# Optimization experiments

Measured on AMD Instinct MI355X. Metric: run time of the kernel, lower is better.

Reference implementation:

```python
import jax, jax.numpy as jnp
import numpy as np

DIM = 1024
D_STATE = 64
D_CONV = 4
EXPAND = 2
D_INNER = DIM * EXPAND          # 2048
N_HEADS = D_INNER // 64         # 32
HEAD_DIM = D_INNER // N_HEADS   # 64
B_SZ = 1
SEQ = 1024
D_IN_PROJ = 2 * D_INNER + 2 * D_STATE + N_HEADS  # 4256
EPS = 1e-6


def setup_inputs() -> dict:
    key = jax.random.key(0)
    ks = jax.random.split(key, 9)
    x = jax.random.normal(ks[0], (B_SZ, SEQ, DIM), jnp.float32)
    W_in = jax.random.normal(ks[1], (D_IN_PROJ, DIM), jnp.float32) / np.sqrt(DIM)
    W_conv = jax.random.normal(ks[2], (D_INNER, 1, D_CONV), jnp.float32) / np.sqrt(D_CONV)
    b_conv = 0.01 * jax.random.normal(ks[3], (D_INNER,), jnp.float32)
    # A_log init: log(arange(1..d_state)) broadcast to (h, d, n), as in the module
    A_log = jnp.log(jnp.arange(1, D_STATE + 1, dtype=jnp.float32)) * jnp.ones((N_HEADS, HEAD_DIM, D_STATE), jnp.float32)
    D = jnp.ones((N_HEADS, HEAD_DIM), jnp.float32) + 0.01 * jax.random.normal(ks[4], (N_HEADS, HEAD_DIM), jnp.float32)
    dt_bias = 0.1 * jax.random.normal(ks[5], (N_HEADS,), jnp.float32)
    norm_w = jnp.ones((D_INNER,), jnp.float32) + 0.01 * jax.random.normal(ks[6], (D_INNER,), jnp.float32)
    W_out = jax.random.normal(ks[7], (DIM, D_INNER), jnp.float32) / np.sqrt(D_INNER)
    return {"x": x, "W_in": W_in, "W_conv": W_conv, "b_conv": b_conv,
            "A_log": A_log, "D": D, "dt_bias": dt_bias, "norm_w": norm_w, "W_out": W_out}


def reference(x, W_in, W_conv, b_conv, A_log, D, dt_bias, norm_w, W_out):
    Bsz, L, _ = x.shape
    zxBCdt = x @ W_in.T  # (B, L, D_IN_PROJ)
    z, xin, Bm, Cm, dt = jnp.split(
        zxBCdt,
        [D_INNER, 2 * D_INNER, 2 * D_INNER + D_STATE, 2 * D_INNER + 2 * D_STATE],
        axis=-1)
    # causal depthwise conv1d (padding d_conv-1 then truncate == left-pad d_conv-1)
    xc = jnp.transpose(xin, (0, 2, 1))  # (B, d_inner, L)
    xc = jax.lax.conv_general_dilated(
        xc, W_conv, window_strides=(1,), padding=[(D_CONV - 1, 0)],
        feature_group_count=D_INNER, dimension_numbers=("NCH", "OIH", "NCH"))
    xc = xc + b_conv[None, :, None]
    xin = jax.nn.silu(jnp.transpose(xc, (0, 2, 1)))  # (B, L, d_inner)
    xh = xin.reshape(Bsz, L, N_HEADS, HEAD_DIM)      # (B, L, h, d)

    A = -jnp.exp(A_log)                     # (h, d, n)
    dt = jax.nn.softplus(dt + dt_bias)      # (B, L, h)

    def step(h_state, ins):
        x_t, dt_t, B_t, C_t = ins  # (B,h,d), (B,h), (B,n), (B,n)
        a = jnp.exp(dt_t[:, :, None, None] * A[None])          # (B,h,d,n)
        h_state = a * h_state + B_t[:, None, None, :] * x_t[..., None]
        y_t = jnp.einsum("bhdn,bn->bhd", h_state, C_t)
        return h_state, y_t

    h0 = jnp.zeros((Bsz, N_HEADS, HEAD_DIM, D_STATE), x.dtype)
    xs = (jnp.moveaxis(xh, 1, 0), jnp.moveaxis(dt, 1, 0),
          jnp.moveaxis(Bm, 1, 0), jnp.moveaxis(Cm, 1, 0))
    _, ys = jax.lax.scan(step, h0, xs)
    y = jnp.moveaxis(ys, 0, 1)              # (B, L, h, d)
    y = y + xh * D[None, None]              # skip term
    y = y.reshape(Bsz, L, D_INNER)
    y = y * jax.nn.silu(z)                  # gating
    rms = jnp.sqrt(jnp.mean(y * y, axis=-1, keepdims=True) + EPS)
    y = y / rms * norm_w                    # RMSNorm
    return y @ W_out.T                      # (B, L, dim)
```

## Files before the change

kernel.cpp:

```cpp
#include <hip/hip_runtime.h>

typedef unsigned short u16;
typedef unsigned int u32;
typedef __attribute__((ext_vector_type(8))) short bf16x8;
typedef __attribute__((ext_vector_type(4))) float f32x4;

#define GPTR(p) ((const __attribute__((address_space(1))) void*)(p))
#define SPTR(p) ((__attribute__((address_space(3))) void*)(p))

#define L_SEQ 1024
#define DIM 1024
#define D_INNER 2048
#define D_STATE 64
#define N_HEADS 32
#define NPROJ 4256
#define NPROJ_PAD 4352
#define COL_Z 0
#define COL_X 2048
#define COL_B 4096
#define COL_C 4160
#define COL_DT 4224
#define NCHUNK 32
#define QCH 32

__device__ __forceinline__ u16 f2bf(float f) {
    unsigned int u = __float_as_uint(f);
    u = u + 0x7fffu + ((u >> 16) & 1u);
    return (u16)(u >> 16);
}
__device__ __forceinline__ float bf2f(u16 h) {
    unsigned int u = ((unsigned int)h) << 16;
    return __uint_as_float(u);
}

__global__ __launch_bounds__(256)
void cast_all_kernel(const float* __restrict__ x, const float* __restrict__ W_in,
                     const float* __restrict__ W_out,
                     u16* __restrict__ xb_hi, u16* __restrict__ xb_lo,
                     u16* __restrict__ Winb, u16* __restrict__ Winb_lo,
                     u16* __restrict__ Woutb)
{
    const int b = blockIdx.x;
    if (b < 1024) {
        const int i = (b * 256 + threadIdx.x) * 4;
        const float4 v = *(const float4*)&x[i];
        const float vs[4] = { v.x, v.y, v.z, v.w };
        u16 oh[4], ol[4];
        #pragma unroll
        for (int j = 0; j < 4; ++j) {
            oh[j] = f2bf(vs[j]);
            ol[j] = f2bf(vs[j] - bf2f(oh[j]));
        }
        *(ushort4*)&xb_hi[i] = *(ushort4*)oh;
        *(ushort4*)&xb_lo[i] = *(ushort4*)ol;
    } else if (b < 5376) {
        const int i = ((b - 1024) * 256 + threadIdx.x) * 4;
        float4 v = make_float4(0.f, 0.f, 0.f, 0.f);
        if (i < NPROJ * DIM) v = *(const float4*)&W_in[i];
        u16 o[4] = { f2bf(v.x), f2bf(v.y), f2bf(v.z), f2bf(v.w) };
        *(ushort4*)&Winb[i] = *(ushort4*)o;
    } else if (b < 5632) {
        const int i = ((b - 5376) * 256 + threadIdx.x) * 4;
        float4 v = make_float4(0.f, 0.f, 0.f, 0.f);
        if (i < (NPROJ - 4096) * DIM) v = *(const float4*)&W_in[(size_t)4096 * DIM + i];
        const float vs[4] = { v.x, v.y, v.z, v.w };
        u16 oh[4], ol[4];
        #pragma unroll
        for (int j = 0; j < 4; ++j) {
            oh[j] = f2bf(vs[j]);
            ol[j] = f2bf(vs[j] - bf2f(oh[j]));
        }
        *(ushort4*)&Winb[(size_t)4096 * DIM + i] = *(ushort4*)oh;
        *(ushort4*)&Winb_lo[i] = *(ushort4*)ol;
    } else {
        const int i = ((b - 5632) * 256 + threadIdx.x) * 4;
        const float4 v = *(const float4*)&W_out[i];
        u16 o[4] = { f2bf(v.x), f2bf(v.y), f2bf(v.z), f2bf(v.w) };
        *(ushort4*)&Woutb[i] = *(ushort4*)o;
    }
}

__global__ __launch_bounds__(256, 2)
void gemm_bt128(const u16* __restrict__ Ah, const u16* __restrict__ Al,
                const u16* __restrict__ Bh, const u16* __restrict__ Bl,
                float* __restrict__ C, int K, int ldc, int precise_from)
{
    __shared__ u16 As[128 * 32];
    __shared__ u16 Bs[128 * 32];
    __shared__ u16 AsL[128 * 32];
    __shared__ u16 BsL[128 * 32];
    const int tid  = threadIdx.x;
    const int wave = tid >> 6;
    const int lane = tid & 63;
    const int row0 = blockIdx.y * 128;
    const int col0 = blockIdx.x * 128;
    const int wm = (wave >> 1) * 64;
    const int wn = (wave & 1) * 64;
    const bool precise = ((int)blockIdx.x >= precise_from);

    f32x4 acc[4][4] = {};

    const int r15 = lane & 15;
    const int ko  = (lane >> 4) * 8;

    for (int kt = 0; kt < K; kt += 32) {
        #pragma unroll
        for (int call = 0; call < 2; ++call) {
            const int ob = call * 4096 + wave * 1024 + lane * 16;
            const int rr = ob >> 6;
            const int kk = (ob & 63) >> 1;
            const size_t goff = (size_t)(row0 + rr) * K + kt + kk;
            const size_t gofb = (size_t)(col0 + rr) * K + kt + kk;
            const int lofs = call * 2048 + wave * 512;
            __builtin_amdgcn_global_load_lds(GPTR(Ah + goff), SPTR(As + lofs), 16, 0, 0);
            __builtin_amdgcn_global_load_lds(GPTR(Bh + gofb), SPTR(Bs + lofs), 16, 0, 0);
            if (precise) {
                __builtin_amdgcn_global_load_lds(GPTR(Al + goff), SPTR(AsL + lofs), 16, 0, 0);
                __builtin_amdgcn_global_load_lds(GPTR(Bl + gofb), SPTR(BsL + lofs), 16, 0, 0);
            }
        }
        __syncthreads();
        bf16x8 av[4], bv[4];
        #pragma unroll
        for (int i = 0; i < 4; ++i)
            av[i] = *(const bf16x8*)&As[(wm + i * 16 + r15) * 32 + ko];
        #pragma unroll
        for (int j = 0; j < 4; ++j)
            bv[j] = *(const bf16x8*)&Bs[(wn + j * 16 + r15) * 32 + ko];
        if (precise) {
            bf16x8 avl[4], bvl[4];
            #pragma unroll
            for (int i = 0; i < 4; ++i)
                avl[i] = *(const bf16x8*)&AsL[(wm + i * 16 + r15) * 32 + ko];
            #pragma unroll
            for (int j = 0; j < 4; ++j)
                bvl[j] = *(const bf16x8*)&BsL[(wn + j * 16 + r15) * 32 + ko];
            #pragma unroll
            for (int i = 0; i < 4; ++i)
                #pragma unroll
                for (int j = 0; j < 4; ++j) {
                    acc[i][j] = __builtin_amdgcn_mfma_f32_16x16x32_bf16(av[i],  bv[j],  acc[i][j], 0, 0, 0);
                    acc[i][j] = __builtin_amdgcn_mfma_f32_16x16x32_bf16(av[i],  bvl[j], acc[i][j], 0, 0, 0);
                    acc[i][j] = __builtin_amdgcn_mfma_f32_16x16x32_bf16(avl[i], bv[j],  acc[i][j], 0, 0, 0);
                }
        } else {
            #pragma unroll
            for (int i = 0; i < 4; ++i)
                #pragma unroll
                for (int j = 0; j < 4; ++j)
                    acc[i][j] = __builtin_amdgcn_mfma_f32_16x16x32_bf16(av[i], bv[j], acc[i][j], 0, 0, 0);
        }
        __syncthreads();
    }

    const int cl = lane & 15;
    const int rg = (lane >> 4) * 4;
    #pragma unroll
    for (int i = 0; i < 4; ++i)
        #pragma unroll
        for (int j = 0; j < 4; ++j)
            #pragma unroll
            for (int reg = 0; reg < 4; ++reg) {
                const int rrow = row0 + wm + i * 16 + rg + reg;
                const int ccol = col0 + wn + j * 16 + cl;
                C[(size_t)rrow * ldc + ccol] = acc[i][j][reg];
            }
}

__global__ __launch_bounds__(256, 2)
void gemm_bt128_sk(const u16* __restrict__ Ah, const u16* __restrict__ Bh,
                   float* __restrict__ Cpart, int Kslice, int lda, int ldb, int ldc)
{
    __shared__ u16 As[128 * 32];
    __shared__ u16 Bs[128 * 32];
    const int tid  = threadIdx.x;
    const int wave = tid >> 6;
    const int lane = tid & 63;
    const int row0 = blockIdx.y * 128;
    const int col0 = blockIdx.x * 128;
    const int wm = (wave >> 1) * 64;
    const int wn = (wave & 1) * 64;
    const int kbase = blockIdx.z * Kslice;
    float* Cp = Cpart + (size_t)blockIdx.z * (1024 * 1024);

    f32x4 acc[4][4] = {};
    const int r15 = lane & 15;
    const int ko  = (lane >> 4) * 8;

    for (int kt = kbase; kt < kbase + Kslice; kt += 32) {
        #pragma unroll
        for (int call = 0; call < 2; ++call) {
            const int ob = call * 4096 + wave * 1024 + lane * 16;
            const int rr = ob >> 6;
            const int kk = (ob & 63) >> 1;
            const int lofs = call * 2048 + wave * 512;
            __builtin_amdgcn_global_load_lds(GPTR(Ah + (size_t)(row0 + rr) * lda + kt + kk),
                                             SPTR(As + lofs), 16, 0, 0);
            __builtin_amdgcn_global_load_lds(GPTR(Bh + (size_t)(col0 + rr) * ldb + kt + kk),
                                             SPTR(Bs + lofs), 16, 0, 0);
        }
        __syncthreads();
        bf16x8 av[4], bv[4];
        #pragma unroll
        for (int i = 0; i < 4; ++i)
            av[i] = *(const bf16x8*)&As[(wm + i * 16 + r15) * 32 + ko];
        #pragma unroll
        for (int j = 0; j < 4; ++j)
            bv[j] = *(const bf16x8*)&Bs[(wn + j * 16 + r15) * 32 + ko];
        #pragma unroll
        for (int i = 0; i < 4; ++i)
            #pragma unroll
            for (int j = 0; j < 4; ++j)
                acc[i][j] = __builtin_amdgcn_mfma_f32_16x16x32_bf16(av[i], bv[j], acc[i][j], 0, 0, 0);
        __syncthreads();
    }

    const int cl = lane & 15;
    const int rg = (lane >> 4) * 4;
    #pragma unroll
    for (int i = 0; i < 4; ++i)
        #pragma unroll
        for (int j = 0; j < 4; ++j)
            #pragma unroll
            for (int reg = 0; reg < 4; ++reg)
                Cp[(size_t)(row0 + wm + i * 16 + rg + reg) * ldc + col0 + wn + j * 16 + cl]
                    = acc[i][j][reg];
}

__global__ __launch_bounds__(256)
void reduce4_kernel(const float* __restrict__ Cpart, float* __restrict__ out)
{
    const int i = (blockIdx.x * 256 + threadIdx.x) * 4;
    const float4 a = *(const float4*)&Cpart[i];
    const float4 b = *(const float4*)&Cpart[i + 1024 * 1024];
    const float4 c = *(const float4*)&Cpart[i + 2 * 1024 * 1024];
    const float4 d = *(const float4*)&Cpart[i + 3 * 1024 * 1024];
    *(float4*)&out[i] = make_float4(a.x + b.x + c.x + d.x, a.y + b.y + c.y + d.y,
                                    a.z + b.z + c.z + d.z, a.w + b.w + c.w + d.w);
}

__global__ __launch_bounds__(256)
void conv_dt_kernel(const float* __restrict__ P,
                    const float* __restrict__ Wc,
                    const float* __restrict__ bc,
                    const float* __restrict__ dtb,
                    const float* __restrict__ A_log,
                    float* __restrict__ xconv,
                    float2* __restrict__ BCp2,
                    float* __restrict__ gT,
                    float* __restrict__ decayT)
{
    const int b = blockIdx.x;
    if (b < 1024) {
        const int t = b;
        const int tid = threadIdx.x;
        const int c0 = tid * 8;
        float acc[8];
        #pragma unroll
        for (int j = 0; j < 8; ++j) acc[j] = bc[c0 + j];
        #pragma unroll
        for (int k = 0; k < 4; ++k) {
            const int tt = t - 3 + k;
            if (tt >= 0) {
                const float* row = P + (size_t)tt * NPROJ_PAD + COL_X + c0;
                float4 a0 = *(const float4*)row;
                float4 a1 = *(const float4*)(row + 4);
                float xv[8] = { a0.x, a0.y, a0.z, a0.w, a1.x, a1.y, a1.z, a1.w };
                #pragma unroll
                for (int j = 0; j < 8; ++j)
                    acc[j] = fmaf(xv[j], Wc[(c0 + j) * 4 + k], acc[j]);
            }
        }
        float o[8];
        #pragma unroll
        for (int j = 0; j < 8; ++j) {
            const float v = acc[j];
            o[j] = v / (1.f + __expf(-v));
        }
        float* dst = xconv + (size_t)t * D_INNER + c0;
        *(float4*)dst       = make_float4(o[0], o[1], o[2], o[3]);
        *(float4*)(dst + 4) = make_float4(o[4], o[5], o[6], o[7]);
        if (tid < 64) {
            const float Bv = P[(size_t)t * NPROJ_PAD + COL_B + tid];
            const float Cv = P[(size_t)t * NPROJ_PAD + COL_C + tid];
            BCp2[t * 64 + tid] = make_float2(Bv, Cv);
        }
    } else {
        const int wv = threadIdx.x >> 6;
        const int lane = threadIdx.x & 63;
        const int idx = (b - 1024) * 4 + wv;
        const int h = idx >> 4;
        const int pr = idx & 15;
        const int t0 = pr * 64;
        float v = P[(size_t)(t0 + lane) * NPROJ_PAD + COL_DT + h] + dtb[h];
        v = (v > 15.f) ? v : __logf(1.f + __expf(v));
        float g = v;
        #pragma unroll
        for (int off = 1; off < 32; off <<= 1) {
            const float u = __shfl_up(g, off);
            if ((lane & 31) >= off) g += u;
        }
        gT[h * L_SEQ + t0 + lane] = g;
        const float Av = -__expf(A_log[(size_t)h * 4096 + lane]);
        #pragma unroll 8
        for (int tt = 0; tt < 64; ++tt) {
            const float dtt = __shfl(v, tt);
            decayT[((size_t)h * L_SEQ + t0 + tt) * 64 + lane] = __expf(dtt * Av);
        }
    }
}

__global__ __launch_bounds__(256)
void xpose_kernel(const float* __restrict__ xconv, float* __restrict__ xT)
{
    __shared__ float tile[64][65];
    const int t0 = blockIdx.x * 64;
    const int c0 = blockIdx.y * 64;
    const int lr = threadIdx.x >> 6;
    const int lc = threadIdx.x & 63;
    #pragma unroll
    for (int r = 0; r < 16; ++r) {
        const int row = r * 4 + lr;
        tile[row][lc] = xconv[(size_t)(t0 + row) * D_INNER + c0 + lc];
    }
    __syncthreads();
    #pragma unroll
    for (int r = 0; r < 16; ++r) {
        const int row = r * 4 + lr;
        xT[(size_t)(c0 + row) * L_SEQ + t0 + lc] = tile[lc][row];
    }
}

__global__ __launch_bounds__(128, 4)
void scan_local_kernel(const float2* __restrict__ BCp2,
                       const float* __restrict__ decayT,
                       const float* __restrict__ xT,
                       float* __restrict__ ygt,
                       u16* __restrict__ S)
{
    __shared__ float2 pt[2][8][2][65];
    const int wv = threadIdx.x >> 6;
    const int lane = threadIdx.x & 63;
    const int hd0 = blockIdx.x * 16 + wv * 8;
    const int pr = blockIdx.y;
    const int h = hd0 >> 6;
    const int tb = pr * 64;

    float sA[8] = {0.f,0.f,0.f,0.f,0.f,0.f,0.f,0.f};
    float sB[8] = {0.f,0.f,0.f,0.f,0.f,0.f,0.f,0.f};

    const float2* bcA = BCp2 + (size_t)tb * 64 + lane;
    const float2* bcB = bcA + 32 * 64;
    const float* dAp = decayT + ((size_t)h * L_SEQ + tb) * 64 + lane;
    const float* dBp = dAp + 32 * 64;
    const float* xr0 = xT + (size_t)hd0 * L_SEQ + tb;

    const int r16 = lane & 15;
    const int seg = lane >> 4;
    const int rd = r16 >> 1;
    const int ri = r16 & 1;

    #pragma unroll
    for (int g = 0; g < 8; ++g) {
        float xA[8][4], xB[8][4];
        #pragma unroll
        for (int d = 0; d < 8; ++d) {
            const float* xr = xr0 + d * L_SEQ;
            const float4 a = *(const float4*)(xr + g * 4);
            const float4 b = *(const float4*)(xr + 32 + g * 4);
            xA[d][0]=a.x; xA[d][1]=a.y; xA[d][2]=a.z; xA[d][3]=a.w;
            xB[d][0]=b.x; xB[d][1]=b.y; xB[d][2]=b.z; xB[d][3]=b.w;
        }
        #pragma unroll
        for (int half = 0; half < 2; ++half) {
            #pragma unroll
            for (int ii2 = 0; ii2 < 2; ++ii2) {
                const int ii = half * 2 + ii2;
                const int i = g * 4 + ii;
                const float2 vA = bcA[i * 64];
                const float2 vB = bcB[i * 64];
                const float aA = dAp[i * 64];
                const float aB = dBp[i * 64];
                #pragma unroll
                for (int d = 0; d < 8; ++d) {
                    sA[d] = fmaf(aA, sA[d], vA.x * xA[d][ii]);
                    sB[d] = fmaf(aB, sB[d], vB.x * xB[d][ii]);
                }
                #pragma unroll
                for (int d = 0; d < 8; ++d)
                    pt[wv][d][ii2][lane] = make_float2(sA[d] * vA.y, sB[d] * vB.y);
            }
            float px = 0.f, py = 0.f;
            #pragma unroll
            for (int k = 0; k < 16; ++k) {
                const float2 v = pt[wv][rd][ri][seg * 16 + k];
                px += v.x; py += v.y;
            }
            px += __shfl_xor(px, 16); py += __shfl_xor(py, 16);
            px += __shfl_xor(px, 32); py += __shfl_xor(py, 32);
            if (lane < 16) {
                const int tA = tb + g * 4 + half * 2 + ri;
                ygt[(size_t)tA * D_INNER + hd0 + rd] = px;
                ygt[(size_t)(tA + 32) * D_INNER + hd0 + rd] = py;
            }
        }
    }
    #pragma unroll
    for (int d = 0; d < 8; ++d) {
        S[((size_t)(hd0 + d) * NCHUNK + pr * 2    ) * 64 + lane] = f2bf(sA[d]);
        S[((size_t)(hd0 + d) * NCHUNK + pr * 2 + 1) * 64 + lane] = f2bf(sB[d]);
    }
}

__global__ __launch_bounds__(256)
void chunk_combine_kernel(const float* __restrict__ A_log,
                          const float* __restrict__ gT,
                          u16* __restrict__ S)
{
    const int tid = blockIdx.x * 256 + threadIdx.x;
    const int hd = tid >> 6;
    const int n  = tid & 63;
    const int h  = hd >> 6;
    const float Av = -__expf(A_log[(size_t)hd * 64 + n]);
    float H = 0.f;
    #pragma unroll 8
    for (int c = 0; c < NCHUNK; ++c) {
        const float Gc = gT[h * L_SEQ + c * QCH + QCH - 1];
        const size_t idx = ((size_t)hd * NCHUNK + c) * 64 + n;
        const float Sl = bf2f(S[idx]);
        S[idx] = f2bf(H);
        H = __expf(Av * Gc) * H + Sl;
    }
}

__global__ __launch_bounds__(256, 2)
void scan_cross_mfma(const float* __restrict__ P,
                     const float* __restrict__ gT,
                     const float* __restrict__ A_log,
                     const u16* __restrict__ S,
                     float* __restrict__ ygt)
{
    const int wv = threadIdx.x >> 6;
    const int lane = threadIdx.x & 63;
    const int idx = blockIdx.x * 4 + wv;
    const int h = idx >> 5;
    const int c = idx & 31;
    const int t0 = c * QCH;
    const int l15 = lane & 15;
    const int lk  = (lane >> 4) * 8;

    float Av8[2][8];
    #pragma unroll
    for (int ss = 0; ss < 2; ++ss)
        #pragma unroll
        for (int qq = 0; qq < 8; ++qq)
            Av8[ss][qq] = -__expf(A_log[(size_t)h * 4096 + ss * 32 + lk + qq]);

    bf16x8 fH[4][2];
    #pragma unroll
    for (int i = 0; i < 4; ++i)
        #pragma unroll
        for (int ss = 0; ss < 2; ++ss)
            fH[i][ss] = *(const bf16x8*)&S[((size_t)(h * 64 + i * 16 + l15) * NCHUNK + c) * 64 + ss * 32 + lk];

    bf16x8 fC[2][2];
    #pragma unroll
    for (int j = 0; j < 2; ++j) {
        const int t = t0 + j * 16 + l15;
        const float g = gT[h * L_SEQ + t];
        #pragma unroll
        for (int ss = 0; ss < 2; ++ss) {
            const float* src = P + (size_t)t * NPROJ_PAD + COL_C + ss * 32 + lk;
            const float4 a = *(const float4*)src;
            const float4 b = *(const float4*)(src + 4);
            const float v[8] = { a.x, a.y, a.z, a.w, b.x, b.y, b.z, b.w };
            bf16x8 rr;
            #pragma unroll
            for (int qq = 0; qq < 8; ++qq)
                rr[qq] = (short)f2bf(v[qq] * __expf(Av8[ss][qq] * g));
            fC[j][ss] = rr;
        }
    }

    f32x4 acc[2][4] = {};
    #pragma unroll
    for (int ss = 0; ss < 2; ++ss)
        #pragma unroll
        for (int j = 0; j < 2; ++j)
            #pragma unroll
            for (int i = 0; i < 4; ++i)
                acc[j][i] = __builtin_amdgcn_mfma_f32_16x16x32_bf16(fC[j][ss], fH[i][ss], acc[j][i], 0, 0, 0);

    const int rg = (lane >> 4) * 4;
    #pragma unroll
    for (int j = 0; j < 2; ++j)
        #pragma unroll
        for (int i = 0; i < 4; ++i)
            #pragma unroll
            for (int rr = 0; rr < 4; ++rr) {
                const int t = t0 + j * 16 + rg + rr;
                const int d = h * 64 + i * 16 + l15;
                ygt[(size_t)t * D_INNER + d] += acc[j][i][rr];
            }
}

__global__ __launch_bounds__(256)
void rmsnorm_kernel(const float* __restrict__ ygt,
                    const float* __restrict__ P,
                    const float* __restrict__ xconv,
                    const float* __restrict__ Dp,
                    const float* __restrict__ nw,
                    u16* __restrict__ Yb)
{
    __shared__ float red[4];
    const int t = blockIdx.x;
    const int tid = threadIdx.x;
    const int c0 = tid * 8;
    const float* zrow = P + (size_t)t * NPROJ_PAD + COL_Z + c0;
    const float4 z0 = *(const float4*)zrow;
    const float4 z1 = *(const float4*)(zrow + 4);
    const float zz[8] = { z0.x, z0.y, z0.z, z0.w, z1.x, z1.y, z1.z, z1.w };
    const float* xrow = xconv + (size_t)t * D_INNER + c0;
    const float4 x0 = *(const float4*)xrow;
    const float4 x1 = *(const float4*)(xrow + 4);
    const float xx[8] = { x0.x, x0.y, x0.z, x0.w, x1.x, x1.y, x1.z, x1.w };
    const float4 d0 = *(const float4*)&Dp[c0];
    const float4 d1 = *(const float4*)&Dp[c0 + 4];
    const float dd[8] = { d0.x, d0.y, d0.z, d0.w, d1.x, d1.y, d1.z, d1.w };
    const float* yrow = ygt + (size_t)t * D_INNER + c0;
    const float4 y0 = *(const float4*)yrow;
    const float4 y1 = *(const float4*)(yrow + 4);
    const float yy[8] = { y0.x, y0.y, y0.z, y0.w, y1.x, y1.y, y1.z, y1.w };
    float v[8];
    float ss = 0.f;
    #pragma unroll
    for (int j = 0; j < 8; ++j) {
        const float yv = yy[j] + dd[j] * xx[j];
        const float z = zz[j];
        const float gated = yv * (z / (1.f + __expf(-z)));
        v[j] = gated;
        ss += gated * gated;
    }
    #pragma unroll
    for (int off = 32; off > 0; off >>= 1) ss += __shfl_xor(ss, off);
    const int wave = tid >> 6;
    if ((tid & 63) == 0) red[wave] = ss;
    __syncthreads();
    const float total = red[0] + red[1] + red[2] + red[3];
    const float scale = rsqrtf(total * (1.f / D_INNER) + 1e-6f);
    u16 o[8];
    #pragma unroll
    for (int j = 0; j < 8; ++j)
        o[j] = f2bf(v[j] * scale * nw[c0 + j]);
    *(uint4*)&Yb[(size_t)t * D_INNER + c0] = *(uint4*)o;
}

extern "C" void kernel_launch(void* const* d_in, const int* in_sizes, int n_in,
                              void* d_out, int out_size, void* d_ws, size_t ws_size,
                              hipStream_t stream)
{
    const float* x      = (const float*)d_in[0];
    const float* W_in   = (const float*)d_in[1];
    const float* W_conv = (const float*)d_in[2];
    const float* b_conv = (const float*)d_in[3];
    const float* A_log  = (const float*)d_in[4];
    const float* Dp     = (const float*)d_in[5];
    const float* dt_bias= (const float*)d_in[6];
    const float* norm_w = (const float*)d_in[7];
    const float* W_out  = (const float*)d_in[8];
    float* out = (float*)d_out;

    char* w = (char*)d_ws;
    u16*   xb_hi  = (u16*)(w);
    u16*   xb_lo  = (u16*)(w + (2u  << 20));
    u16*   Winb   = (u16*)(w + (4u  << 20));
    u16*   Winb_lo= (u16*)(w + (12u << 20) + (512u << 10));
    float* decayT = (float*)(w);
    u16*   Yb     = (u16*)(w);
    u16*   S      = (u16*)(w + (8u  << 20));
    u16*   Woutb  = (u16*)(w + (16u << 20));
    float* P      = (float*)(w + (20u << 20));
    float* Cpart  = (float*)(w + (20u << 20));
    float* xconv  = (float*)(w + (37u << 20));
    float* gT     = (float*)(w + (45u << 20));
    float2* BCp2  = (float2*)(w + (45u << 20) + (512u << 10));
    float* ygt    = (float*)(w + (46u << 20));
    float* xT     = (float*)(w + (54u << 20));

    const u16* Winb_lo_virt = Winb_lo - (size_t)4096 * DIM;

    cast_all_kernel<<<dim3(7680), 256, 0, stream>>>(
        x, W_in, W_out, xb_hi, xb_lo, Winb, Winb_lo, Woutb);

    gemm_bt128<<<dim3(NPROJ_PAD / 128, L_SEQ / 128), 256, 0, stream>>>(
        xb_hi, xb_lo, Winb, Winb_lo_virt, P, DIM, NPROJ_PAD, 32);

    conv_dt_kernel<<<dim3(1024 + 128), 256, 0, stream>>>(
        P, W_conv, b_conv, dt_bias, A_log, xconv, BCp2, gT, decayT);

    xpose_kernel<<<dim3(L_SEQ / 64, D_INNER / 64), 256, 0, stream>>>(xconv, xT);

    scan_local_kernel<<<dim3(D_INNER / 16, 16), 128, 0, stream>>>(
        BCp2, decayT, xT, ygt, S);
    chunk_combine_kernel<<<dim3(D_INNER * 64 / 256), 256, 0, stream>>>(A_log, gT, S);
    scan_cross_mfma<<<dim3(N_HEADS * NCHUNK / 4), 256, 0, stream>>>(P, gT, A_log, S, ygt);

    rmsnorm_kernel<<<dim3(L_SEQ), 256, 0, stream>>>(ygt, P, xconv, Dp, norm_w, Yb);

    gemm_bt128_sk<<<dim3(DIM / 128, L_SEQ / 128, 4), 256, 0, stream>>>(
        Yb, Woutb, Cpart, D_INNER / 4, D_INNER, D_INNER, DIM);
    reduce4_kernel<<<dim3(DIM * L_SEQ / 4 / 256), 256, 0, stream>>>(Cpart, out);
}
```

Measured before the change: 155.3 us.

## Double-buffer LDS tiles in both GEMM kernels to overlap loads with MFMA

Both GEMM kernels now use two LDS buffers per operand and issue the global-to-LDS loads for tile k+1 before computing on tile k. The aim is to hide global memory latency behind the MFMA work instead of stalling at each barrier. This doubles LDS use per block (up to 64KB in the precise kernel), which may lower occupancy. There is also only one barrier per iteration, and the compiler may insert a vmcnt wait that serializes the prefetch anyway.

Result: no change. 157.5 us (+1.4%).

```diff
diff --git a/kernel.cpp b/kernel.cpp
--- a/kernel.cpp
+++ b/kernel.cpp
@@ -85,10 +85,10 @@
                 const u16* __restrict__ Bh, const u16* __restrict__ Bl,
                 float* __restrict__ C, int K, int ldc, int precise_from)
 {
-    __shared__ u16 As[128 * 32];
-    __shared__ u16 Bs[128 * 32];
-    __shared__ u16 AsL[128 * 32];
-    __shared__ u16 BsL[128 * 32];
+    __shared__ u16 As[2][128 * 32];
+    __shared__ u16 Bs[2][128 * 32];
+    __shared__ u16 AsL[2][128 * 32];
+    __shared__ u16 BsL[2][128 * 32];
     const int tid  = threadIdx.x;
     const int wave = tid >> 6;
     const int lane = tid & 63;
@@ -103,7 +103,7 @@
     const int r15 = lane & 15;
     const int ko  = (lane >> 4) * 8;
 
-    for (int kt = 0; kt < K; kt += 32) {
+    auto stage = [&](int buf, int kt) {
         #pragma unroll
         for (int call = 0; call < 2; ++call) {
             const int ob = call * 4096 + wave * 1024 + lane * 16;
@@ -112,29 +112,36 @@
             const size_t goff = (size_t)(row0 + rr) * K + kt + kk;
             const size_t gofb = (size_t)(col0 + rr) * K + kt + kk;
             const int lofs = call * 2048 + wave * 512;
-            __builtin_amdgcn_global_load_lds(GPTR(Ah + goff), SPTR(As + lofs), 16, 0, 0);
-            __builtin_amdgcn_global_load_lds(GPTR(Bh + gofb), SPTR(Bs + lofs), 16, 0, 0);
+            __builtin_amdgcn_global_load_lds(GPTR(Ah + goff), SPTR(&As[buf][lofs]), 16, 0, 0);
+            __builtin_amdgcn_global_load_lds(GPTR(Bh + gofb), SPTR(&Bs[buf][lofs]), 16, 0, 0);
             if (precise) {
-                __builtin_amdgcn_global_load_lds(GPTR(Al + goff), SPTR(AsL + lofs), 16, 0, 0);
-                __builtin_amdgcn_global_load_lds(GPTR(Bl + gofb), SPTR(BsL + lofs), 16, 0, 0);
+                __builtin_amdgcn_global_load_lds(GPTR(Al + goff), SPTR(&AsL[buf][lofs]), 16, 0, 0);
+                __builtin_amdgcn_global_load_lds(GPTR(Bl + gofb), SPTR(&BsL[buf][lofs]), 16, 0, 0);
             }
         }
-        __syncthreads();
+    };
+
+    stage(0, 0);
+    __syncthreads();
+    int cur = 0;
+    const int nt = K / 32;
+    for (int it = 0; it < nt; ++it) {
+        if (it + 1 < nt) stage(cur ^ 1, (it + 1) * 32);
         bf16x8 av[4], bv[4];
         #pragma unroll
         for (int i = 0; i < 4; ++i)
-            av[i] = *(const bf16x8*)&As[(wm + i * 16 + r15) * 32 + ko];
+            av[i] = *(const bf16x8*)&As[cur][(wm + i * 16 + r15) * 32 + ko];
         #pragma unroll
         for (int j = 0; j < 4; ++j)
-            bv[j] = *(const bf16x8*)&Bs[(wn + j * 16 + r15) * 32 + ko];
+            bv[j] = *(const bf16x8*)&Bs[cur][(wn + j * 16 + r15) * 32 + ko];
         if (precise) {
             bf16x8 avl[4], bvl[4];
             #pragma unroll
             for (int i = 0; i < 4; ++i)
-                avl[i] = *(const bf16x8*)&AsL[(wm + i * 16 + r15) * 32 + ko];
+                avl[i] = *(const bf16x8*)&AsL[cur][(wm + i * 16 + r15) * 32 + ko];
             #pragma unroll
             for (int j = 0; j < 4; ++j)
-                bvl[j] = *(const bf16x8*)&BsL[(wn + j * 16 + r15) * 32 + ko];
+                bvl[j] = *(const bf16x8*)&BsL[cur][(wn + j * 16 + r15) * 32 + ko];
             #pragma unroll
             for (int i = 0; i < 4; ++i)
                 #pragma unroll
@@ -151,6 +158,7 @@
                     acc[i][j] = __builtin_amdgcn_mfma_f32_16x16x32_bf16(av[i], bv[j], acc[i][j], 0, 0, 0);
         }
         __syncthreads();
+        cur ^= 1;
     }
 
     const int cl = lane & 15;
@@ -171,8 +179,8 @@
 void gemm_bt128_sk(const u16* __restrict__ Ah, const u16* __restrict__ Bh,
                    float* __restrict__ Cpart, int Kslice, int lda, int ldb, int ldc)
 {
-    __shared__ u16 As[128 * 32];
-    __shared__ u16 Bs[128 * 32];
+    __shared__ u16 As[2][128 * 32];
+    __shared__ u16 Bs[2][128 * 32];
     const int tid  = threadIdx.x;
     const int wave = tid >> 6;
     const int lane = tid & 63;
@@ -187,7 +195,7 @@
     const int r15 = lane & 15;
     const int ko  = (lane >> 4) * 8;
 
-    for (int kt = kbase; kt < kbase + Kslice; kt += 32) {
+    auto stage = [&](int buf, int kt) {
         #pragma unroll
         for (int call = 0; call < 2; ++call) {
             const int ob = call * 4096 + wave * 1024 + lane * 16;
@@ -195,24 +203,32 @@
             const int kk = (ob & 63) >> 1;
             const int lofs = call * 2048 + wave * 512;
             __builtin_amdgcn_global_load_lds(GPTR(Ah + (size_t)(row0 + rr) * lda + kt + kk),
-                                             SPTR(As + lofs), 16, 0, 0);
+                                             SPTR(&As[buf][lofs]), 16, 0, 0);
             __builtin_amdgcn_global_load_lds(GPTR(Bh + (size_t)(col0 + rr) * ldb + kt + kk),
-                                             SPTR(Bs + lofs), 16, 0, 0);
-        }
-        __syncthreads();
+                                             SPTR(&Bs[buf][lofs]), 16, 0, 0);
+        }
+    };
+
+    stage(0, kbase);
+    __syncthreads();
+    int cur = 0;
+    const int nt = Kslice / 32;
+    for (int it = 0; it < nt; ++it) {
+        if (it + 1 < nt) stage(cur ^ 1, kbase + (it + 1) * 32);
         bf16x8 av[4], bv[4];
         #pragma unroll
         for (int i = 0; i < 4; ++i)
-            av[i] = *(const bf16x8*)&As[(wm + i * 16 + r15) * 32 + ko];
+            av[i] = *(const bf16x8*)&As[cur][(wm + i * 16 + r15) * 32 + ko];
         #pragma unroll
         for (int j = 0; j < 4; ++j)
-            bv[j] = *(const bf16x8*)&Bs[(wn + j * 16 + r15) * 32 + ko];
+            bv[j] = *(const bf16x8*)&Bs[cur][(wn + j * 16 + r15) * 32 + ko];
         #pragma unroll
         for (int i = 0; i < 4; ++i)
             #pragma unroll
             for (int j = 0; j < 4; ++j)
                 acc[i][j] = __builtin_amdgcn_mfma_f32_16x16x32_bf16(av[i], bv[j], acc[i][j], 0, 0, 0);
         __syncthreads();
+        cur ^= 1;
     }
 
     const int cl = lane & 15;
```
